# Kernel tuning notes

Hardware: AMD Instinct MI355X
Metric: run time of the kernel (lower is better)

The kernel has to match this reference:

```python
import jax, jax.numpy as jnp
import numpy as np

T, B, I, H, K = 200, 2048, 128, 128, 4


def setup_inputs() -> dict:
    key = jax.random.key(0)
    ks = jax.random.split(key, 7)
    inputs = jax.random.normal(ks[0], (T, B, I), jnp.float32)
    lengths = jax.random.randint(ks[1], (B,), 1, T + 1, jnp.int32)
    si = 1.0 / np.sqrt(I)
    sh = 1.0 / np.sqrt(H)
    w0 = jax.random.uniform(ks[2], (H,), jnp.float32, -sh, sh)      # Linear(H,1,bias=False)
    w1_w = jax.random.uniform(ks[3], (H, I), jnp.float32, -si, si)  # Linear(I,H)
    w1_b = jax.random.uniform(ks[4], (H,), jnp.float32, -si, si)
    w2_w = jax.random.uniform(ks[5], (H, I), jnp.float32, -si, si)  # Linear(I,H,bias=False)
    w3_w = jax.random.uniform(ks[6], (H, I), jnp.float32, -si, si)  # Linear(I,H,bias=False)
    return dict(inputs=inputs, lengths=lengths, label_len=4,
                w0=w0, w1_w=w1_w, w1_b=w1_b, w2_w=w2_w, w3_w=w3_w)


def reference(inputs, lengths, label_len, w0, w1_w, w1_b, w2_w, w3_w):
    # inputs: [T, B, I] time-major padded sequences; lengths: [B]
    T_, B_, _ = inputs.shape
    Kl = label_len
    dt = inputs.dtype
    # packed semantics: padded positions are exactly zero
    valid = (jnp.arange(T_)[:, None] < lengths[None, :])  # [T, B]
    x = inputs * valid[..., None].astype(dt)
    x1 = x @ w1_w.T + w1_b                                 # [T, B, H]
    x2 = x @ w2_w.T                                        # [T, B, H]
    # running mean m_s[t] = mean(inputs[:t+1]) (zeros at padding, as in torch)
    m_s = jnp.cumsum(x, axis=0) / jnp.arange(1, T_ + 1, dtype=dt)[:, None, None]
    # labeled timesteps: last min(L, label_len) steps of each sequence
    start = jnp.maximum(lengths - Kl, 0)                   # [B]
    t_lab = start[:, None] + jnp.arange(Kl)[None, :]       # [B, K]
    lab_valid = t_lab < lengths[:, None]                   # [B, K]
    t_c = jnp.minimum(t_lab, T_ - 1)
    b_idx = jnp.arange(B_)[:, None]
    x2_lab = x2[t_c, b_idx]                                # [B, K, H]
    wms_lab = m_s[t_c, b_idx] @ w3_w.T                     # [B, K, H]
    c = x2_lab + wms_lab                                   # [B, K, H]
    # att[b,k,s] = w0 . sigmoid(x1[s,b] + x2[t_k,b] + wms[t_k,b])
    att = jnp.einsum('sbkh,h->bks',
                     jax.nn.sigmoid(x1[:, :, None, :] + c[None, :, :, :]), w0)
    causal = (jnp.arange(T_)[None, None, :] <= t_lab[:, :, None]) & lab_valid[:, :, None]
    att = att * causal.astype(dt)                          # [B, K, T]
    h = jnp.einsum('bks,sbh->bkh', att, x1) + x2_lab       # [B, K, H]
    return h * lab_valid[..., None].astype(dt)
```

## Files before the change

### kernel.cpp

```cpp
#include <hip/hip_runtime.h>
#include <stdint.h>

#define T_DIM 200
#define B_DIM 2048
#define I_DIM 128
#define H_DIM 128
#define TS    16
#define XST   201

typedef float  f32x4  __attribute__((ext_vector_type(4)));
typedef __bf16 bf16x8 __attribute__((ext_vector_type(8)));

union BF8 { ushort4 u2[2]; bf16x8 v; };

static __device__ __forceinline__ unsigned short f2bf(float f) {
    union { float f; unsigned u; } c; c.f = f;
    unsigned u = c.u + (0x7FFFu + ((c.u >> 16) & 1u));
    return (unsigned short)(u >> 16);
}
static __device__ __forceinline__ float bf2f(unsigned short s) {
    union { unsigned u; float f; } c; c.u = ((unsigned)s) << 16;
    return c.f;
}

__global__ __launch_bounds__(256) void fused_kernel(
    const float* __restrict__ x, const int* __restrict__ lengths,
    const float* __restrict__ w0, const float* __restrict__ w1,
    const float* __restrict__ b1, const float* __restrict__ w2,
    const float* __restrict__ w3, float* __restrict__ out)
{
    __shared__ __align__(16) unsigned short xs[TS][136];
    __shared__ __align__(16) unsigned short x1t[H_DIM][XST];
    __shared__ __align__(16) unsigned short axl[4][136];
    __shared__ __align__(16) unsigned short ams[4][136];
    __shared__ __align__(16) float ekt[H_DIM][4];
    __shared__ __align__(16) float x2ls[4][H_DIM];
    __shared__ __align__(16) float attk[XST][4];

    const int b    = blockIdx.x;
    const int tid  = threadIdx.x;
    const int lane = tid & 63;
    const int wv   = tid >> 6;
    const int l15  = lane & 15;
    const int quad = lane >> 4;
    const int L     = lengths[b];
    const int start = (L > 4) ? (L - 4) : 0;
    const int nv    = (L < 4) ? L : 4;

    bf16x8 bfr[2][4];
    float  bias[2];
    #pragma unroll
    for (int nt = 0; nt < 2; ++nt) {
        const int n = wv * 32 + nt * 16 + l15;
        bias[nt] = b1[n];
        #pragma unroll
        for (int ks = 0; ks < 4; ++ks) {
            const int kc = ks * 32 + quad * 8;
            const float4 p0 = *(const float4*)(w1 + (size_t)n * I_DIM + kc);
            const float4 p1 = *(const float4*)(w1 + (size_t)n * I_DIM + kc + 4);
            BF8 t;
            t.u2[0] = make_ushort4(f2bf(p0.x), f2bf(p0.y), f2bf(p0.z), f2bf(p0.w));
            t.u2[1] = make_ushort4(f2bf(p1.x), f2bf(p1.y), f2bf(p1.z), f2bf(p1.w));
            bfr[nt][ks] = t.v;
        }
    }

    float p = 0.f;
    float ps0 = 0.f, ps1 = 0.f, ps2 = 0.f, ps3 = 0.f;
    unsigned short xl0 = 0, xl1 = 0, xl2 = 0, xl3 = 0;

    for (int t0 = 0; t0 < L; t0 += TS) {
        const int nrows = (L - t0 < TS) ? (L - t0) : TS;
        #pragma unroll
        for (int it = 0; it < 2; ++it) {
            const int sl = tid + it * 256;
            const int r = sl >> 5, f4 = sl & 31;
            if (r < nrows) {
                const float4 v = *(const float4*)(
                    x + ((size_t)(t0 + r) * B_DIM + b) * I_DIM + f4 * 4);
                *(ushort4*)(&xs[r][f4 * 4]) =
                    make_ushort4(f2bf(v.x), f2bf(v.y), f2bf(v.z), f2bf(v.w));
            }
        }
        __syncthreads();

        if (tid < 128) {
            const int s0 = start - t0;
            for (int r = 0; r < nrows; ++r) {
                const unsigned short raw = xs[r][tid];
                p += bf2f(raw);
                if (r == s0    ) { ps0 = p; xl0 = raw; }
                if (r == s0 + 1) { ps1 = p; xl1 = raw; }
                if (r == s0 + 2) { ps2 = p; xl2 = raw; }
                if (r == s0 + 3) { ps3 = p; xl3 = raw; }
            }
        }

        bf16x8 afr[4];
        #pragma unroll
        for (int ks = 0; ks < 4; ++ks)
            afr[ks] = *(const bf16x8*)&xs[l15][ks * 32 + quad * 8];
        #pragma unroll
        for (int nt = 0; nt < 2; ++nt) {
            f32x4 acc = (f32x4){0.f, 0.f, 0.f, 0.f};
            #pragma unroll
            for (int ks = 0; ks < 4; ++ks)
                acc = __builtin_amdgcn_mfma_f32_16x16x32_bf16(afr[ks], bfr[nt][ks], acc, 0, 0, 0);
            const int h  = wv * 32 + nt * 16 + l15;
            const int tb = t0 + quad * 4;
            #pragma unroll
            for (int r = 0; r < 4; ++r) {
                const int t = tb + r;
                if (t - t0 < nrows) x1t[h][t] = f2bf(acc[r] + bias[nt]);
            }
        }
        __syncthreads();
    }

    if (tid < 128) {
        axl[0][tid] = xl0; axl[1][tid] = xl1; axl[2][tid] = xl2; axl[3][tid] = xl3;
        ams[0][tid] = f2bf(ps0 / (float)(start + 1));
        ams[1][tid] = f2bf(ps1 / (float)(start + 2));
        ams[2][tid] = f2bf(ps2 / (float)(start + 3));
        ams[3][tid] = f2bf(ps3 / (float)(start + 4));
    }
    __syncthreads();

    #pragma unroll
    for (int nt = 0; nt < 2; ++nt) {
        const int n = wv * 32 + nt * 16 + l15;
        f32x4 c1 = (f32x4){0.f, 0.f, 0.f, 0.f};
        f32x4 c2 = (f32x4){0.f, 0.f, 0.f, 0.f};
        #pragma unroll
        for (int ks = 0; ks < 4; ++ks) {
            const int kc = ks * 32 + quad * 8;
            const bf16x8 a1 = *(const bf16x8*)&axl[l15 & 3][kc];
            const bf16x8 a2 = *(const bf16x8*)&ams[l15 & 3][kc];
            const float4 q0 = *(const float4*)(w2 + (size_t)n * I_DIM + kc);
            const float4 q1 = *(const float4*)(w2 + (size_t)n * I_DIM + kc + 4);
            const float4 r0 = *(const float4*)(w3 + (size_t)n * I_DIM + kc);
            const float4 r1 = *(const float4*)(w3 + (size_t)n * I_DIM + kc + 4);
            BF8 bw2, bw3;
            bw2.u2[0] = make_ushort4(f2bf(q0.x), f2bf(q0.y), f2bf(q0.z), f2bf(q0.w));
            bw2.u2[1] = make_ushort4(f2bf(q1.x), f2bf(q1.y), f2bf(q1.z), f2bf(q1.w));
            bw3.u2[0] = make_ushort4(f2bf(r0.x), f2bf(r0.y), f2bf(r0.z), f2bf(r0.w));
            bw3.u2[1] = make_ushort4(f2bf(r1.x), f2bf(r1.y), f2bf(r1.z), f2bf(r1.w));
            c1 = __builtin_amdgcn_mfma_f32_16x16x32_bf16(a1, bw2.v, c1, 0, 0, 0);
            c2 = __builtin_amdgcn_mfma_f32_16x16x32_bf16(a2, bw3.v, c2, 0, 0, 0);
        }
        if (quad == 0) {
            #pragma unroll
            for (int r = 0; r < 4; ++r) {
                x2ls[r][n] = c1[r];
                ekt[n][r]  = __builtin_amdgcn_exp2f(-1.44269504f * (c1[r] + c2[r]));
            }
        }
    }
    __syncthreads();

    const int s = tid;
    if (s < L) {
        float a0 = 0.f, a1 = 0.f, a2 = 0.f, a3 = 0.f;
        #pragma unroll 8
        for (int h = 0; h < H_DIM; ++h) {
            const float xv = bf2f(x1t[h][s]);
            const float E  = __builtin_amdgcn_exp2f(-1.44269504f * xv);
            const f32x4 ek = *(const f32x4*)&ekt[h][0];
            const float wh = w0[h];
            a0 += wh * __builtin_amdgcn_rcpf(1.f + E * ek[0]);
            a1 += wh * __builtin_amdgcn_rcpf(1.f + E * ek[1]);
            a2 += wh * __builtin_amdgcn_rcpf(1.f + E * ek[2]);
            a3 += wh * __builtin_amdgcn_rcpf(1.f + E * ek[3]);
        }
        attk[s][0] = (0 < nv && s <= start    ) ? a0 : 0.f;
        attk[s][1] = (1 < nv && s <= start + 1) ? a1 : 0.f;
        attk[s][2] = (2 < nv && s <= start + 2) ? a2 : 0.f;
        attk[s][3] = (3 < nv && s <= start + 3) ? a3 : 0.f;
    }
    __syncthreads();

    const int h    = tid & 127;
    const int half = tid >> 7;
    const int Lh   = (L + 1) >> 1;
    const int ssb  = half ? Lh : 0;
    const int sse  = half ? L  : Lh;
    float h0 = 0.f, h1 = 0.f, h2 = 0.f, h3 = 0.f;
    #pragma unroll 4
    for (int ss = ssb; ss < sse; ++ss) {
        const f32x4 a4 = *(const f32x4*)&attk[ss][0];
        const float xv = bf2f(x1t[h][ss]);
        h0 += a4[0] * xv; h1 += a4[1] * xv; h2 += a4[2] * xv; h3 += a4[3] * xv;
    }
    float* hacc2 = (float*)&ekt[0][0];
    if (half) {
        hacc2[h * 4 + 0] = h0; hacc2[h * 4 + 1] = h1;
        hacc2[h * 4 + 2] = h2; hacc2[h * 4 + 3] = h3;
    }
    __syncthreads();
    if (tid < 128) {
        h0 += hacc2[h * 4 + 0]; h1 += hacc2[h * 4 + 1];
        h2 += hacc2[h * 4 + 2]; h3 += hacc2[h * 4 + 3];
        out[((size_t)b * 4 + 0) * H_DIM + h] = (0 < nv) ? h0 + x2ls[0][h] : 0.f;
        out[((size_t)b * 4 + 1) * H_DIM + h] = (1 < nv) ? h1 + x2ls[1][h] : 0.f;
        out[((size_t)b * 4 + 2) * H_DIM + h] = (2 < nv) ? h2 + x2ls[2][h] : 0.f;
        out[((size_t)b * 4 + 3) * H_DIM + h] = (3 < nv) ? h3 + x2ls[3][h] : 0.f;
    }
}

extern "C" void kernel_launch(void* const* d_in, const int* in_sizes, int n_in,
                              void* d_out, int out_size, void* d_ws, size_t ws_size,
                              hipStream_t stream) {
    (void)in_sizes; (void)n_in; (void)out_size; (void)d_ws; (void)ws_size;
    const float* x       = (const float*)d_in[0];
    const int*   lengths = (const int*)d_in[1];
    const float* w0 = (const float*)d_in[3];
    const float* w1 = (const float*)d_in[4];
    const float* b1 = (const float*)d_in[5];
    const float* w2 = (const float*)d_in[6];
    const float* w3 = (const float*)d_in[7];
    float* out = (float*)d_out;

    fused_kernel<<<dim3(B_DIM), 256, 0, stream>>>(x, lengths, w0, w1, b1, w2, w3, out);
}
```

Before: 402.9 us.

## Stream x1 tiles through LDS and fuse attention into the tile loop

The kernel no longer keeps the full per-sequence x1 matrix in shared memory. It computes the running-mean prefix sums in a separate fp32 pass over global x, then loops over 32-step tiles. Each tile runs the x1 MFMA, the sigmoid attention spread across all 256 threads, and the weighted accumulation of h. This cuts LDS use sharply, aiming for more resident blocks per CU (launch_bounds now requests 4) and better thread utilisation in the attention stage. In exchange it reads x twice, once for the prefix pass and once for the tiles, and adds more barriers per tile.

```diff
diff --git a/kernel.cpp b/kernel.cpp
--- a/kernel.cpp
+++ b/kernel.cpp
@@ -5,8 +5,7 @@
 #define B_DIM 2048
 #define I_DIM 128
 #define H_DIM 128
-#define TS    16
-#define XST   201
+#define TS    32
 
 typedef float  f32x4  __attribute__((ext_vector_type(4)));
 typedef __bf16 bf16x8 __attribute__((ext_vector_type(8)));
@@ -23,19 +22,21 @@
     return c.f;
 }
 
-__global__ __launch_bounds__(256) void fused_kernel(
+__global__ __launch_bounds__(256, 4) void fused_kernel(
     const float* __restrict__ x, const int* __restrict__ lengths,
     const float* __restrict__ w0, const float* __restrict__ w1,
     const float* __restrict__ b1, const float* __restrict__ w2,
     const float* __restrict__ w3, float* __restrict__ out)
 {
     __shared__ __align__(16) unsigned short xs[TS][136];
-    __shared__ __align__(16) unsigned short x1t[H_DIM][XST];
+    __shared__ __align__(16) unsigned short x1s[TS][130];
+    __shared__ __align__(16) float attp[TS][36];
+    __shared__ __align__(16) float attk[TS][4];
+    __shared__ __align__(16) float ektL[H_DIM][4];
+    __shared__ __align__(16) float x2ls[4][H_DIM];
+    __shared__ __align__(16) float w0s[H_DIM];
     __shared__ __align__(16) unsigned short axl[4][136];
     __shared__ __align__(16) unsigned short ams[4][136];
-    __shared__ __align__(16) float ekt[H_DIM][4];
-    __shared__ __align__(16) float x2ls[4][H_DIM];
-    __shared__ __align__(16) float attk[XST][4];
 
     const int b    = blockIdx.x;
     const int tid  = threadIdx.x;
@@ -47,6 +48,8 @@
     const int start = (L > 4) ? (L - 4) : 0;
     const int nv    = (L < 4) ? L : 4;
 
+    if (tid < 128) w0s[tid] = w0[tid];
+
     bf16x8 bfr[2][4];
     float  bias[2];
     #pragma unroll
@@ -65,64 +68,42 @@
         }
     }
 
-    float p = 0.f;
-    float ps0 = 0.f, ps1 = 0.f, ps2 = 0.f, ps3 = 0.f;
-    unsigned short xl0 = 0, xl1 = 0, xl2 = 0, xl3 = 0;
-
-    for (int t0 = 0; t0 < L; t0 += TS) {
-        const int nrows = (L - t0 < TS) ? (L - t0) : TS;
-        #pragma unroll
-        for (int it = 0; it < 2; ++it) {
-            const int sl = tid + it * 256;
-            const int r = sl >> 5, f4 = sl & 31;
-            if (r < nrows) {
-                const float4 v = *(const float4*)(
-                    x + ((size_t)(t0 + r) * B_DIM + b) * I_DIM + f4 * 4);
-                *(ushort4*)(&xs[r][f4 * 4]) =
-                    make_ushort4(f2bf(v.x), f2bf(v.y), f2bf(v.z), f2bf(v.w));
-            }
-        }
-        __syncthreads();
-
-        if (tid < 128) {
-            const int s0 = start - t0;
-            for (int r = 0; r < nrows; ++r) {
-                const unsigned short raw = xs[r][tid];
-                p += bf2f(raw);
-                if (r == s0    ) { ps0 = p; xl0 = raw; }
-                if (r == s0 + 1) { ps1 = p; xl1 = raw; }
-                if (r == s0 + 2) { ps2 = p; xl2 = raw; }
-                if (r == s0 + 3) { ps3 = p; xl3 = raw; }
-            }
-        }
-
-        bf16x8 afr[4];
-        #pragma unroll
-        for (int ks = 0; ks < 4; ++ks)
-            afr[ks] = *(const bf16x8*)&xs[l15][ks * 32 + quad * 8];
-        #pragma unroll
-        for (int nt = 0; nt < 2; ++nt) {
-            f32x4 acc = (f32x4){0.f, 0.f, 0.f, 0.f};
-            #pragma unroll
-            for (int ks = 0; ks < 4; ++ks)
-                acc = __builtin_amdgcn_mfma_f32_16x16x32_bf16(afr[ks], bfr[nt][ks], acc, 0, 0, 0);
-            const int h  = wv * 32 + nt * 16 + l15;
-            const int tb = t0 + quad * 4;
-            #pragma unroll
-            for (int r = 0; r < 4; ++r) {
-                const int t = tb + r;
-                if (t - t0 < nrows) x1t[h][t] = f2bf(acc[r] + bias[nt]);
-            }
-        }
-        __syncthreads();
-    }
+    const int i    = tid & 127;
+    const int half = tid >> 7;
+    const int m    = start >> 1;
+    const float* xp = x + (size_t)b * I_DIM + i;
+    {
+        const int tb = half ? m : 0;
+        const int te = half ? start : m;
+        float s = 0.f;
+        int t = tb;
+        for (; t + 4 <= te; t += 4) {
+            const float a0 = xp[(size_t)(t + 0) * (B_DIM * I_DIM)];
+            const float a1 = xp[(size_t)(t + 1) * (B_DIM * I_DIM)];
+            const float a2 = xp[(size_t)(t + 2) * (B_DIM * I_DIM)];
+            const float a3 = xp[(size_t)(t + 3) * (B_DIM * I_DIM)];
+            s += a0 + a1 + a2 + a3;
+        }
+        for (; t < te; ++t) s += xp[(size_t)t * (B_DIM * I_DIM)];
+        float* psum = &attp[0][0];
+        psum[half * 128 + i] = s;
+    }
+    __syncthreads();
 
     if (tid < 128) {
-        axl[0][tid] = xl0; axl[1][tid] = xl1; axl[2][tid] = xl2; axl[3][tid] = xl3;
-        ams[0][tid] = f2bf(ps0 / (float)(start + 1));
-        ams[1][tid] = f2bf(ps1 / (float)(start + 2));
-        ams[2][tid] = f2bf(ps2 / (float)(start + 3));
-        ams[3][tid] = f2bf(ps3 / (float)(start + 4));
+        float* psum = &attp[0][0];
+        float p = psum[i] + psum[128 + i];
+        const float v0 = xp[(size_t)(start + 0) * (B_DIM * I_DIM)];
+        const float v1 = xp[(size_t)(start + 1) * (B_DIM * I_DIM)];
+        const float v2 = xp[(size_t)(start + 2) * (B_DIM * I_DIM)];
+        const float v3 = xp[(size_t)(start + 3) * (B_DIM * I_DIM)];
+        const float p0 = p + v0, p1 = p0 + v1, p2 = p1 + v2, p3 = p2 + v3;
+        axl[0][i] = f2bf(v0); axl[1][i] = f2bf(v1);
+        axl[2][i] = f2bf(v2); axl[3][i] = f2bf(v3);
+        ams[0][i] = f2bf(p0 / (float)(start + 1));
+        ams[1][i] = f2bf(p1 / (float)(start + 2));
+        ams[2][i] = f2bf(p2 / (float)(start + 3));
+        ams[3][i] = f2bf(p3 / (float)(start + 4));
     }
     __syncthreads();
 
@@ -152,58 +133,122 @@
             #pragma unroll
             for (int r = 0; r < 4; ++r) {
                 x2ls[r][n] = c1[r];
-                ekt[n][r]  = __builtin_amdgcn_exp2f(-1.44269504f * (c1[r] + c2[r]));
+                ektL[n][r] = __builtin_amdgcn_exp2f(-1.44269504f * (c1[r] + c2[r]));
             }
         }
     }
     __syncthreads();
 
-    const int s = tid;
-    if (s < L) {
-        float a0 = 0.f, a1 = 0.f, a2 = 0.f, a3 = 0.f;
-        #pragma unroll 8
-        for (int h = 0; h < H_DIM; ++h) {
-            const float xv = bf2f(x1t[h][s]);
-            const float E  = __builtin_amdgcn_exp2f(-1.44269504f * xv);
-            const f32x4 ek = *(const f32x4*)&ekt[h][0];
-            const float wh = w0[h];
-            a0 += wh * __builtin_amdgcn_rcpf(1.f + E * ek[0]);
-            a1 += wh * __builtin_amdgcn_rcpf(1.f + E * ek[1]);
-            a2 += wh * __builtin_amdgcn_rcpf(1.f + E * ek[2]);
-            a3 += wh * __builtin_amdgcn_rcpf(1.f + E * ek[3]);
-        }
-        attk[s][0] = (0 < nv && s <= start    ) ? a0 : 0.f;
-        attk[s][1] = (1 < nv && s <= start + 1) ? a1 : 0.f;
-        attk[s][2] = (2 < nv && s <= start + 2) ? a2 : 0.f;
-        attk[s][3] = (3 < nv && s <= start + 3) ? a3 : 0.f;
-    }
-    __syncthreads();
-
-    const int h    = tid & 127;
-    const int half = tid >> 7;
-    const int Lh   = (L + 1) >> 1;
-    const int ssb  = half ? Lh : 0;
-    const int sse  = half ? L  : Lh;
-    float h0 = 0.f, h1 = 0.f, h2 = 0.f, h3 = 0.f;
-    #pragma unroll 4
-    for (int ss = ssb; ss < sse; ++ss) {
-        const f32x4 a4 = *(const f32x4*)&attk[ss][0];
-        const float xv = bf2f(x1t[h][ss]);
-        h0 += a4[0] * xv; h1 += a4[1] * xv; h2 += a4[2] * xv; h3 += a4[3] * xv;
-    }
-    float* hacc2 = (float*)&ekt[0][0];
-    if (half) {
-        hacc2[h * 4 + 0] = h0; hacc2[h * 4 + 1] = h1;
-        hacc2[h * 4 + 2] = h2; hacc2[h * 4 + 3] = h3;
-    }
-    __syncthreads();
-    if (tid < 128) {
-        h0 += hacc2[h * 4 + 0]; h1 += hacc2[h * 4 + 1];
-        h2 += hacc2[h * 4 + 2]; h3 += hacc2[h * 4 + 3];
-        out[((size_t)b * 4 + 0) * H_DIM + h] = (0 < nv) ? h0 + x2ls[0][h] : 0.f;
-        out[((size_t)b * 4 + 1) * H_DIM + h] = (1 < nv) ? h1 + x2ls[1][h] : 0.f;
-        out[((size_t)b * 4 + 2) * H_DIM + h] = (2 < nv) ? h2 + x2ls[2][h] : 0.f;
-        out[((size_t)b * 4 + 3) * H_DIM + h] = (3 < nv) ? h3 + x2ls[3][h] : 0.f;
+    const int sq = tid & 31;
+    const int hg = tid >> 5;
+    const int hcol = tid & 127;
+    float hacc0 = 0.f, hacc1 = 0.f, hacc2v = 0.f, hacc3 = 0.f;
+
+    for (int t0 = 0; t0 < L; t0 += TS) {
+        const int nrows = (L - t0 < TS) ? (L - t0) : TS;
+
+        #pragma unroll
+        for (int it = 0; it < 4; ++it) {
+            const int sl = tid + it * 256;
+            const int r = sl >> 5, f4 = sl & 31;
+            ushort4 w = make_ushort4(0, 0, 0, 0);
+            if (r < nrows) {
+                const float4 v = *(const float4*)(
+                    x + ((size_t)(t0 + r) * B_DIM + b) * I_DIM + f4 * 4);
+                w = make_ushort4(f2bf(v.x), f2bf(v.y), f2bf(v.z), f2bf(v.w));
+            }
+            *(ushort4*)&xs[r][f4 * 4] = w;
+        }
+        __syncthreads();
+
+        #pragma unroll
+        for (int mt = 0; mt < 2; ++mt) {
+            bf16x8 afr[4];
+            #pragma unroll
+            for (int ks = 0; ks < 4; ++ks)
+                afr[ks] = *(const bf16x8*)&xs[mt * 16 + l15][ks * 32 + quad * 8];
+            #pragma unroll
+            for (int nt = 0; nt < 2; ++nt) {
+                f32x4 acc = (f32x4){0.f, 0.f, 0.f, 0.f};
+                #pragma unroll
+                for (int ks = 0; ks < 4; ++ks)
+                    acc = __builtin_amdgcn_mfma_f32_16x16x32_bf16(
+                        afr[ks], bfr[nt][ks], acc, 0, 0, 0);
+                const int h = wv * 32 + nt * 16 + l15;
+                const int tr = mt * 16 + quad * 4;
+                #pragma unroll
+                for (int r = 0; r < 4; ++r)
+                    x1s[tr + r][h] = f2bf(acc[r] + bias[nt]);
+            }
+        }
+        __syncthreads();
+
+        {
+            const int h0 = hg * 16;
+            f32x4 a = (f32x4){0.f, 0.f, 0.f, 0.f};
+            #pragma unroll
+            for (int hh = 0; hh < 16; hh += 2) {
+                const int h = h0 + hh;
+                const unsigned xv2 = *(const unsigned*)&x1s[sq][h];
+                const float xa = bf2f((unsigned short)(xv2 & 0xFFFFu));
+                const float xb = bf2f((unsigned short)(xv2 >> 16));
+                const float Ea = __builtin_amdgcn_exp2f(-1.44269504f * xa);
+                const float Eb = __builtin_amdgcn_exp2f(-1.44269504f * xb);
+                const f32x4 eka = *(const f32x4*)&ektL[h][0];
+                const f32x4 ekb = *(const f32x4*)&ektL[h + 1][0];
+                const float wa = w0s[h], wb = w0s[h + 1];
+                #pragma unroll
+                for (int k = 0; k < 4; ++k)
+                    a[k] += wa * __builtin_amdgcn_rcpf(1.f + Ea * eka[k])
+                          + wb * __builtin_amdgcn_rcpf(1.f + Eb * ekb[k]);
+            }
+            *(f32x4*)&attp[sq][hg * 4] = a;
+        }
+        __syncthreads();
+
+        if (tid < TS) {
+            const int s = t0 + tid;
+            f32x4 sm = (f32x4){0.f, 0.f, 0.f, 0.f};
+            #pragma unroll
+            for (int g = 0; g < 8; ++g)
+                sm += *(const f32x4*)&attp[tid][g * 4];
+            f32x4 o;
+            o[0] = (0 < nv && s <= start    ) ? sm[0] : 0.f;
+            o[1] = (1 < nv && s <= start + 1) ? sm[1] : 0.f;
+            o[2] = (2 < nv && s <= start + 2) ? sm[2] : 0.f;
+            o[3] = (3 < nv && s <= start + 3) ? sm[3] : 0.f;
+            *(f32x4*)&attk[tid][0] = o;
+        }
+        __syncthreads();
+
+        {
+            const int sbase = half * 16;
+            #pragma unroll
+            for (int s2 = 0; s2 < 16; ++s2) {
+                const int srow = sbase + s2;
+                const f32x4 a4 = *(const f32x4*)&attk[srow][0];
+                const float xv = bf2f(x1s[srow][hcol]);
+                hacc0 += a4[0] * xv; hacc1 += a4[1] * xv;
+                hacc2v += a4[2] * xv; hacc3 += a4[3] * xv;
+            }
+        }
+        __syncthreads();
+    }
+
+    {
+        float* h2 = &attp[0][0];
+        if (half == 1) {
+            *(f32x4*)&h2[hcol * 4] = (f32x4){hacc0, hacc1, hacc2v, hacc3};
+        }
+        __syncthreads();
+        if (tid < 128) {
+            const f32x4 o = *(const f32x4*)&h2[hcol * 4];
+            hacc0 += o[0]; hacc1 += o[1]; hacc2v += o[2]; hacc3 += o[3];
+            out[((size_t)b * 4 + 0) * H_DIM + hcol] = (0 < nv) ? hacc0 + x2ls[0][hcol] : 0.f;
+            out[((size_t)b * 4 + 1) * H_DIM + hcol] = (1 < nv) ? hacc1 + x2ls[1][hcol] : 0.f;
+            out[((size_t)b * 4 + 2) * H_DIM + hcol] = (2 < nv) ? hacc2v + x2ls[2][hcol] : 0.f;
+            out[((size_t)b * 4 + 3) * H_DIM + hcol] = (3 < nv) ? hacc3 + x2ls[3][hcol] : 0.f;
+        }
     }
 }
 
```

Result: faster. 386.6 us (-4.1%).

## Stream x1 tiles through registers and fuse attention and output accumulation per tile

Applied to the files above, without the earlier changes.

The kernel no longer stores the full x1 matrix transposed in shared memory. It first computes the prefix sum and the labelled rows directly from global memory, using wave-parallel partial sums. It then streams x in 16-row tiles, computes x1 with MFMA, evaluates the sigmoid attention in registers, reduces across lanes with shuffles and shared-memory atomics into a double-buffered attention tile, and accumulates h in registers. This removes the large x1t/attk shared buffers and raises occupancy, with launch bounds set to 4 blocks per CU. In exchange, x is read twice from global memory (once for the prefix sum, once for the tiles), and each tile now needs two barriers plus atomics.

```diff
diff --git a/kernel.cpp b/kernel.cpp
--- a/kernel.cpp
+++ b/kernel.cpp
@@ -6,7 +6,6 @@
 #define I_DIM 128
 #define H_DIM 128
 #define TS    16
-#define XST   201
 
 typedef float  f32x4  __attribute__((ext_vector_type(4)));
 typedef __bf16 bf16x8 __attribute__((ext_vector_type(8)));
@@ -22,20 +21,24 @@
     union { unsigned u; float f; } c; c.u = ((unsigned)s) << 16;
     return c.f;
 }
-
-__global__ __launch_bounds__(256) void fused_kernel(
+static __device__ __forceinline__ bf16x8 cvt8(const float4 a, const float4 b) {
+    BF8 t;
+    t.u2[0] = make_ushort4(f2bf(a.x), f2bf(a.y), f2bf(a.z), f2bf(a.w));
+    t.u2[1] = make_ushort4(f2bf(b.x), f2bf(b.y), f2bf(b.z), f2bf(b.w));
+    return t.v;
+}
+
+__global__ __launch_bounds__(256, 4) void fused_kernel(
     const float* __restrict__ x, const int* __restrict__ lengths,
     const float* __restrict__ w0, const float* __restrict__ w1,
     const float* __restrict__ b1, const float* __restrict__ w2,
     const float* __restrict__ w3, float* __restrict__ out)
 {
-    __shared__ __align__(16) unsigned short xs[TS][136];
-    __shared__ __align__(16) unsigned short x1t[H_DIM][XST];
-    __shared__ __align__(16) unsigned short axl[4][136];
-    __shared__ __align__(16) unsigned short ams[4][136];
-    __shared__ __align__(16) float ekt[H_DIM][4];
-    __shared__ __align__(16) float x2ls[4][H_DIM];
-    __shared__ __align__(16) float attk[XST][4];
+    __shared__ __align__(16) float psum[4][128];
+    __shared__ __align__(16) unsigned short axl[4][132];
+    __shared__ __align__(16) unsigned short ams[4][132];
+    __shared__ __align__(16) float ektL[H_DIM][4];
+    __shared__ __align__(16) float attk[2][TS][4];
 
     const int b    = blockIdx.x;
     const int tid  = threadIdx.x;
@@ -46,89 +49,71 @@
     const int L     = lengths[b];
     const int start = (L > 4) ? (L - 4) : 0;
     const int nv    = (L < 4) ? L : 4;
+    const int hbase = wv * 32;
+
+    if (tid < 128) ((float*)attk)[tid] = 0.f;
 
     bf16x8 bfr[2][4];
-    float  bias[2];
+    float  biasr[2], w0r[2];
     #pragma unroll
     for (int nt = 0; nt < 2; ++nt) {
-        const int n = wv * 32 + nt * 16 + l15;
-        bias[nt] = b1[n];
+        const int n = hbase + nt * 16 + l15;
+        biasr[nt] = b1[n];
+        w0r[nt]   = w0[n];
         #pragma unroll
         for (int ks = 0; ks < 4; ++ks) {
             const int kc = ks * 32 + quad * 8;
-            const float4 p0 = *(const float4*)(w1 + (size_t)n * I_DIM + kc);
-            const float4 p1 = *(const float4*)(w1 + (size_t)n * I_DIM + kc + 4);
-            BF8 t;
-            t.u2[0] = make_ushort4(f2bf(p0.x), f2bf(p0.y), f2bf(p0.z), f2bf(p0.w));
-            t.u2[1] = make_ushort4(f2bf(p1.x), f2bf(p1.y), f2bf(p1.z), f2bf(p1.w));
-            bfr[nt][ks] = t.v;
-        }
-    }
-
-    float p = 0.f;
-    float ps0 = 0.f, ps1 = 0.f, ps2 = 0.f, ps3 = 0.f;
-    unsigned short xl0 = 0, xl1 = 0, xl2 = 0, xl3 = 0;
-
-    for (int t0 = 0; t0 < L; t0 += TS) {
-        const int nrows = (L - t0 < TS) ? (L - t0) : TS;
-        #pragma unroll
-        for (int it = 0; it < 2; ++it) {
-            const int sl = tid + it * 256;
-            const int r = sl >> 5, f4 = sl & 31;
-            if (r < nrows) {
-                const float4 v = *(const float4*)(
-                    x + ((size_t)(t0 + r) * B_DIM + b) * I_DIM + f4 * 4);
-                *(ushort4*)(&xs[r][f4 * 4]) =
-                    make_ushort4(f2bf(v.x), f2bf(v.y), f2bf(v.z), f2bf(v.w));
-            }
-        }
-        __syncthreads();
-
-        if (tid < 128) {
-            const int s0 = start - t0;
-            for (int r = 0; r < nrows; ++r) {
-                const unsigned short raw = xs[r][tid];
-                p += bf2f(raw);
-                if (r == s0    ) { ps0 = p; xl0 = raw; }
-                if (r == s0 + 1) { ps1 = p; xl1 = raw; }
-                if (r == s0 + 2) { ps2 = p; xl2 = raw; }
-                if (r == s0 + 3) { ps3 = p; xl3 = raw; }
-            }
-        }
-
-        bf16x8 afr[4];
-        #pragma unroll
-        for (int ks = 0; ks < 4; ++ks)
-            afr[ks] = *(const bf16x8*)&xs[l15][ks * 32 + quad * 8];
-        #pragma unroll
-        for (int nt = 0; nt < 2; ++nt) {
-            f32x4 acc = (f32x4){0.f, 0.f, 0.f, 0.f};
-            #pragma unroll
-            for (int ks = 0; ks < 4; ++ks)
-                acc = __builtin_amdgcn_mfma_f32_16x16x32_bf16(afr[ks], bfr[nt][ks], acc, 0, 0, 0);
-            const int h  = wv * 32 + nt * 16 + l15;
-            const int tb = t0 + quad * 4;
-            #pragma unroll
-            for (int r = 0; r < 4; ++r) {
-                const int t = tb + r;
-                if (t - t0 < nrows) x1t[h][t] = f2bf(acc[r] + bias[nt]);
-            }
-        }
-        __syncthreads();
-    }
+            bfr[nt][ks] = cvt8(*(const float4*)(w1 + (size_t)n * I_DIM + kc),
+                               *(const float4*)(w1 + (size_t)n * I_DIM + kc + 4));
+        }
+    }
+
+    {
+        const int q  = (start + 3) >> 2;
+        const int tb = wv * q;
+        const int te = (tb + q < start) ? (tb + q) : start;
+        const float* xb2 = x + (size_t)b * I_DIM + 2 * lane;
+        float s0 = 0.f, s1 = 0.f;
+        int t = tb;
+        for (; t + 4 <= te; t += 4) {
+            const float2 a0 = *(const float2*)(xb2 + (size_t)(t + 0) * (B_DIM * I_DIM));
+            const float2 a1 = *(const float2*)(xb2 + (size_t)(t + 1) * (B_DIM * I_DIM));
+            const float2 a2 = *(const float2*)(xb2 + (size_t)(t + 2) * (B_DIM * I_DIM));
+            const float2 a3 = *(const float2*)(xb2 + (size_t)(t + 3) * (B_DIM * I_DIM));
+            s0 += a0.x + a1.x + a2.x + a3.x;
+            s1 += a0.y + a1.y + a2.y + a3.y;
+        }
+        for (; t < te; ++t) {
+            const float2 a = *(const float2*)(xb2 + (size_t)t * (B_DIM * I_DIM));
+            s0 += a.x; s1 += a.y;
+        }
+        psum[wv][2 * lane]     = s0;
+        psum[wv][2 * lane + 1] = s1;
+    }
+    __syncthreads();
 
     if (tid < 128) {
-        axl[0][tid] = xl0; axl[1][tid] = xl1; axl[2][tid] = xl2; axl[3][tid] = xl3;
-        ams[0][tid] = f2bf(ps0 / (float)(start + 1));
-        ams[1][tid] = f2bf(ps1 / (float)(start + 2));
-        ams[2][tid] = f2bf(ps2 / (float)(start + 3));
-        ams[3][tid] = f2bf(ps3 / (float)(start + 4));
+        const int i = tid;
+        float p = psum[0][i] + psum[1][i] + psum[2][i] + psum[3][i];
+        const float* xi = x + (size_t)b * I_DIM + i;
+        const float v0 = xi[(size_t)(start + 0) * (B_DIM * I_DIM)];
+        const float v1 = xi[(size_t)(start + 1) * (B_DIM * I_DIM)];
+        const float v2 = xi[(size_t)(start + 2) * (B_DIM * I_DIM)];
+        const float v3 = xi[(size_t)(start + 3) * (B_DIM * I_DIM)];
+        const float p0 = p + v0, p1 = p0 + v1, p2 = p1 + v2, p3 = p2 + v3;
+        axl[0][i] = f2bf(v0); axl[1][i] = f2bf(v1);
+        axl[2][i] = f2bf(v2); axl[3][i] = f2bf(v3);
+        ams[0][i] = f2bf(p0 / (float)(start + 1));
+        ams[1][i] = f2bf(p1 / (float)(start + 2));
+        ams[2][i] = f2bf(p2 / (float)(start + 3));
+        ams[3][i] = f2bf(p3 / (float)(start + 4));
     }
     __syncthreads();
 
+    f32x4 x2lr[2];
     #pragma unroll
     for (int nt = 0; nt < 2; ++nt) {
-        const int n = wv * 32 + nt * 16 + l15;
+        const int n = hbase + nt * 16 + l15;
         f32x4 c1 = (f32x4){0.f, 0.f, 0.f, 0.f};
         f32x4 c2 = (f32x4){0.f, 0.f, 0.f, 0.f};
         #pragma unroll
@@ -136,74 +121,126 @@
             const int kc = ks * 32 + quad * 8;
             const bf16x8 a1 = *(const bf16x8*)&axl[l15 & 3][kc];
             const bf16x8 a2 = *(const bf16x8*)&ams[l15 & 3][kc];
-            const float4 q0 = *(const float4*)(w2 + (size_t)n * I_DIM + kc);
-            const float4 q1 = *(const float4*)(w2 + (size_t)n * I_DIM + kc + 4);
-            const float4 r0 = *(const float4*)(w3 + (size_t)n * I_DIM + kc);
-            const float4 r1 = *(const float4*)(w3 + (size_t)n * I_DIM + kc + 4);
-            BF8 bw2, bw3;
-            bw2.u2[0] = make_ushort4(f2bf(q0.x), f2bf(q0.y), f2bf(q0.z), f2bf(q0.w));
-            bw2.u2[1] = make_ushort4(f2bf(q1.x), f2bf(q1.y), f2bf(q1.z), f2bf(q1.w));
-            bw3.u2[0] = make_ushort4(f2bf(r0.x), f2bf(r0.y), f2bf(r0.z), f2bf(r0.w));
-            bw3.u2[1] = make_ushort4(f2bf(r1.x), f2bf(r1.y), f2bf(r1.z), f2bf(r1.w));
-            c1 = __builtin_amdgcn_mfma_f32_16x16x32_bf16(a1, bw2.v, c1, 0, 0, 0);
-            c2 = __builtin_amdgcn_mfma_f32_16x16x32_bf16(a2, bw3.v, c2, 0, 0, 0);
-        }
+            const bf16x8 b2 = cvt8(*(const float4*)(w2 + (size_t)n * I_DIM + kc),
+                                   *(const float4*)(w2 + (size_t)n * I_DIM + kc + 4));
+            const bf16x8 b3 = cvt8(*(const float4*)(w3 + (size_t)n * I_DIM + kc),
+                                   *(const float4*)(w3 + (size_t)n * I_DIM + kc + 4));
+            c1 = __builtin_amdgcn_mfma_f32_16x16x32_bf16(a1, b2, c1, 0, 0, 0);
+            c2 = __builtin_amdgcn_mfma_f32_16x16x32_bf16(a2, b3, c2, 0, 0, 0);
+        }
+        x2lr[nt] = c1;
         if (quad == 0) {
+            f32x4 e;
+            #pragma unroll
+            for (int k = 0; k < 4; ++k)
+                e[k] = __builtin_amdgcn_exp2f(-1.44269504f * (c1[k] + c2[k]));
+            *(f32x4*)&ektL[n][0] = e;
+        }
+    }
+    __syncthreads();
+
+    f32x4 ektr[2];
+    #pragma unroll
+    for (int nt = 0; nt < 2; ++nt)
+        ektr[nt] = *(const f32x4*)&ektL[hbase + nt * 16 + l15][0];
+
+    float hacc[2][4];
+    #pragma unroll
+    for (int nt = 0; nt < 2; ++nt)
+        #pragma unroll
+        for (int k = 0; k < 4; ++k) hacc[nt][k] = 0.f;
+
+    int parity = 0;
+    for (int t0 = 0; t0 < L; t0 += TS, parity ^= 1) {
+        const int  row  = t0 + l15;
+        const bool vrow = row < L;
+        const int  ra   = vrow ? row : (L - 1);
+        const float* xr = x + ((size_t)ra * B_DIM + b) * I_DIM + quad * 8;
+        bf16x8 afr[4];
+        #pragma unroll
+        for (int ks = 0; ks < 4; ++ks) {
+            float4 p0 = *(const float4*)(xr + ks * 32);
+            float4 p1 = *(const float4*)(xr + ks * 32 + 4);
+            if (!vrow) { p0 = make_float4(0, 0, 0, 0); p1 = make_float4(0, 0, 0, 0); }
+            afr[ks] = cvt8(p0, p1);
+        }
+
+        float x1c[2][4];
+        #pragma unroll
+        for (int nt = 0; nt < 2; ++nt) {
+            f32x4 acc = (f32x4){0.f, 0.f, 0.f, 0.f};
+            #pragma unroll
+            for (int ks = 0; ks < 4; ++ks)
+                acc = __builtin_amdgcn_mfma_f32_16x16x32_bf16(afr[ks], bfr[nt][ks], acc, 0, 0, 0);
+            #pragma unroll
+            for (int r = 0; r < 4; ++r) x1c[nt][r] = acc[r] + biasr[nt];
+        }
+
+        float part[4][4];
+        #pragma unroll
+        for (int r = 0; r < 4; ++r) {
+            #pragma unroll
+            for (int k = 0; k < 4; ++k) part[r][k] = 0.f;
+            #pragma unroll
+            for (int nt = 0; nt < 2; ++nt) {
+                const float E = __builtin_amdgcn_exp2f(-1.44269504f * x1c[nt][r]);
+                #pragma unroll
+                for (int k = 0; k < 4; ++k)
+                    part[r][k] += w0r[nt] * __builtin_amdgcn_rcpf(1.f + E * ektr[nt][k]);
+            }
+        }
+        #pragma unroll
+        for (int m = 1; m <= 8; m <<= 1)
+            #pragma unroll
+            for (int r = 0; r < 4; ++r)
+                #pragma unroll
+                for (int k = 0; k < 4; ++k)
+                    part[r][k] += __shfl_xor(part[r][k], m);
+
+        if (l15 == 0) {
             #pragma unroll
             for (int r = 0; r < 4; ++r) {
-                x2ls[r][n] = c1[r];
-                ekt[n][r]  = __builtin_amdgcn_exp2f(-1.44269504f * (c1[r] + c2[r]));
+                const int s = t0 + quad * 4 + r;
+                #pragma unroll
+                for (int k = 0; k < 4; ++k) {
+                    const float v = (k < nv && s <= start + k) ? part[r][k] : 0.f;
+                    atomicAdd(&attk[parity][quad * 4 + r][k], v);
+                }
             }
         }
-    }
-    __syncthreads();
-
-    const int s = tid;
-    if (s < L) {
-        float a0 = 0.f, a1 = 0.f, a2 = 0.f, a3 = 0.f;
-        #pragma unroll 8
-        for (int h = 0; h < H_DIM; ++h) {
-            const float xv = bf2f(x1t[h][s]);
-            const float E  = __builtin_amdgcn_exp2f(-1.44269504f * xv);
-            const f32x4 ek = *(const f32x4*)&ekt[h][0];
-            const float wh = w0[h];
-            a0 += wh * __builtin_amdgcn_rcpf(1.f + E * ek[0]);
-            a1 += wh * __builtin_amdgcn_rcpf(1.f + E * ek[1]);
-            a2 += wh * __builtin_amdgcn_rcpf(1.f + E * ek[2]);
-            a3 += wh * __builtin_amdgcn_rcpf(1.f + E * ek[3]);
-        }
-        attk[s][0] = (0 < nv && s <= start    ) ? a0 : 0.f;
-        attk[s][1] = (1 < nv && s <= start + 1) ? a1 : 0.f;
-        attk[s][2] = (2 < nv && s <= start + 2) ? a2 : 0.f;
-        attk[s][3] = (3 < nv && s <= start + 3) ? a3 : 0.f;
-    }
-    __syncthreads();
-
-    const int h    = tid & 127;
-    const int half = tid >> 7;
-    const int Lh   = (L + 1) >> 1;
-    const int ssb  = half ? Lh : 0;
-    const int sse  = half ? L  : Lh;
-    float h0 = 0.f, h1 = 0.f, h2 = 0.f, h3 = 0.f;
-    #pragma unroll 4
-    for (int ss = ssb; ss < sse; ++ss) {
-        const f32x4 a4 = *(const f32x4*)&attk[ss][0];
-        const float xv = bf2f(x1t[h][ss]);
-        h0 += a4[0] * xv; h1 += a4[1] * xv; h2 += a4[2] * xv; h3 += a4[3] * xv;
-    }
-    float* hacc2 = (float*)&ekt[0][0];
-    if (half) {
-        hacc2[h * 4 + 0] = h0; hacc2[h * 4 + 1] = h1;
-        hacc2[h * 4 + 2] = h2; hacc2[h * 4 + 3] = h3;
-    }
-    __syncthreads();
-    if (tid < 128) {
-        h0 += hacc2[h * 4 + 0]; h1 += hacc2[h * 4 + 1];
-        h2 += hacc2[h * 4 + 2]; h3 += hacc2[h * 4 + 3];
-        out[((size_t)b * 4 + 0) * H_DIM + h] = (0 < nv) ? h0 + x2ls[0][h] : 0.f;
-        out[((size_t)b * 4 + 1) * H_DIM + h] = (1 < nv) ? h1 + x2ls[1][h] : 0.f;
-        out[((size_t)b * 4 + 2) * H_DIM + h] = (2 < nv) ? h2 + x2ls[2][h] : 0.f;
-        out[((size_t)b * 4 + 3) * H_DIM + h] = (3 < nv) ? h3 + x2ls[3][h] : 0.f;
+        __syncthreads();
+
+        #pragma unroll
+        for (int r = 0; r < 4; ++r) {
+            const f32x4 a4 = *(const f32x4*)&attk[parity][quad * 4 + r][0];
+            #pragma unroll
+            for (int nt = 0; nt < 2; ++nt)
+                #pragma unroll
+                for (int k = 0; k < 4; ++k)
+                    hacc[nt][k] += a4[k] * x1c[nt][r];
+        }
+        if (tid < 64) ((float*)&attk[parity ^ 1][0][0])[tid] = 0.f;
+        __syncthreads();
+    }
+
+    #pragma unroll
+    for (int nt = 0; nt < 2; ++nt)
+        #pragma unroll
+        for (int k = 0; k < 4; ++k) {
+            float v = hacc[nt][k];
+            v += __shfl_xor(v, 16);
+            v += __shfl_xor(v, 32);
+            hacc[nt][k] = v;
+        }
+    if (quad == 0) {
+        #pragma unroll
+        for (int nt = 0; nt < 2; ++nt) {
+            const int h = hbase + nt * 16 + l15;
+            #pragma unroll
+            for (int k = 0; k < 4; ++k)
+                out[((size_t)b * 4 + k) * H_DIM + h] =
+                    (k < nv) ? (hacc[nt][k] + x2lr[nt][k]) : 0.f;
+        }
     }
 }
 
```

After: 388.4 us. 3.6% less time.
